# Optimization experiments

Hardware: AMD Instinct MI355X
Metric: run time of the kernel (lower is better)

## Reference

```python
import jax, jax.numpy as jnp
import numpy as np

B = 65536
D_IN = 512
H = 512
EPS = 1e-5


def _layernorm(x, gamma, beta):
    # matches torch ref: unbiased std (ddof=1), eps added to std (not var)
    mean = jnp.mean(x, axis=-1, keepdims=True)
    std = jnp.std(x, axis=-1, ddof=1, keepdims=True)
    return gamma * (x - mean) / (std + EPS) + beta


def setup_inputs() -> dict:
    key = jax.random.key(0)
    ks = jax.random.split(key, 16)
    fan_in = D_IN + H
    s = 1.0 / np.sqrt(fan_in)
    inp = {
        "x": jax.random.normal(ks[0], (B, D_IN), dtype=jnp.float32),
        "prev_h": jax.random.normal(ks[1], (B, H), dtype=jnp.float32),
        "prev_c": jax.random.normal(ks[2], (B, H), dtype=jnp.float32),
        # torch Linear: weight [out, in], bias [out]
        "Wf": jax.random.uniform(ks[3], (H, fan_in), jnp.float32, -s, s),
        "bf": jax.random.uniform(ks[4], (H,), jnp.float32, -s, s),
        "Wi": jax.random.uniform(ks[5], (H, fan_in), jnp.float32, -s, s),
        "bi": jax.random.uniform(ks[6], (H,), jnp.float32, -s, s),
        "Wo": jax.random.uniform(ks[7], (H, fan_in), jnp.float32, -s, s),
        "bo": jax.random.uniform(ks[8], (H,), jnp.float32, -s, s),
        "Wj": jax.random.uniform(ks[9], (H, fan_in), jnp.float32, -s, s),
        "bj": jax.random.uniform(ks[10], (H,), jnp.float32, -s, s),
        "gamma_f": jnp.ones((H,), jnp.float32),
        "beta_f": jnp.zeros((H,), jnp.float32),
        "gamma_i": jnp.ones((H,), jnp.float32),
        "beta_i": jnp.zeros((H,), jnp.float32),
        "gamma_o": jnp.ones((H,), jnp.float32),
        "beta_o": jnp.zeros((H,), jnp.float32),
        "gamma_j": jnp.ones((H,), jnp.float32),
        "beta_j": jnp.zeros((H,), jnp.float32),
        "gamma_c": jnp.ones((H,), jnp.float32),
        "beta_c": jnp.zeros((H,), jnp.float32),
    }
    return inp


def reference(x, prev_h, prev_c, Wf, bf, Wi, bi, Wo, bo, Wj, bj,
              gamma_f, beta_f, gamma_i, beta_i, gamma_o, beta_o,
              gamma_j, beta_j, gamma_c, beta_c):
    combined = jnp.concatenate([x, prev_h], axis=-1)  # [B, D_IN+H]
    ft = jax.nn.sigmoid(_layernorm(combined @ Wf.T + bf, gamma_f, beta_f))
    it = jax.nn.sigmoid(_layernorm(combined @ Wi.T + bi, gamma_i, beta_i))
    ot = jax.nn.sigmoid(_layernorm(combined @ Wo.T + bo, gamma_o, beta_o))
    jt = jnp.tanh(_layernorm(combined @ Wj.T + bj, gamma_j, beta_j))
    c = ft * prev_c + jnp.minimum(1.0 - ft, it) * jt
    c = _layernorm(c, gamma_c, beta_c)
    h = ot * c
    return (h, c)
```

## Files before the change

### kernel.cpp

```cpp
#include <hip/hip_runtime.h>
#include <math.h>

#define B_ROWS 65536
#define D_IN   512
#define HDIM   512
#define FAN    1024
#define NCOL   2048
#define EPS    1e-5f

#define BM 256
#define BN 256
#define BK 64
#define KTILES (FAN / BK)
#define NITER  (KTILES / 2)

typedef unsigned short u16;
using bfrag = __attribute__((ext_vector_type(8))) short;
using facc  = __attribute__((ext_vector_type(4))) float;
using us4   = __attribute__((ext_vector_type(4))) unsigned short;
using us8   = __attribute__((ext_vector_type(8))) unsigned short;

static __device__ __forceinline__ u16 f2b(float f) {
    unsigned u = __builtin_bit_cast(unsigned, f);
    u += 0x7fffu + ((u >> 16) & 1u);
    return (u16)(u >> 16);
}
static __device__ __forceinline__ float b2f(u16 h) {
    unsigned u = ((unsigned)h) << 16;
    return __builtin_bit_cast(float, u);
}
static __device__ __forceinline__ void gload16(const u16* g, u16* l) {
    __builtin_amdgcn_global_load_lds(
        (const __attribute__((address_space(1))) void*)g,
        (__attribute__((address_space(3))) void*)l, 16, 0, 0);
}

__global__ void pack_combined(const float* __restrict__ x, const float* __restrict__ ph,
                              u16* __restrict__ comb)
{
    long i = (long)blockIdx.x * 256 + threadIdx.x;
    if (i >= (long)B_ROWS * D_IN / 4) return;
    long e = i * 4;
    long b = e >> 9;
    int  d = (int)(e & 511);
    float4 xv = *(const float4*)(x + e);
    float4 hv = *(const float4*)(ph + e);
    us4 xb = { f2b(xv.x), f2b(xv.y), f2b(xv.z), f2b(xv.w) };
    us4 hb = { f2b(hv.x), f2b(hv.y), f2b(hv.z), f2b(hv.w) };
    *(us4*)(comb + b * FAN + d)        = xb;
    *(us4*)(comb + b * FAN + D_IN + d) = hb;
}

__global__ void pack_w(const float* __restrict__ Wf, const float* __restrict__ Wi,
                       const float* __restrict__ Wo, const float* __restrict__ Wj,
                       u16* __restrict__ Wall)
{
    long i = (long)blockIdx.x * 256 + threadIdx.x;
    if (i >= (long)NCOL * FAN / 4) return;
    long e = i * 4;
    int  g = (int)(e >> 19);
    long rem = e & 524287L;
    const float* src = (g == 0) ? Wf : (g == 1) ? Wi : (g == 2) ? Wo : Wj;
    float4 v = *(const float4*)(src + rem);
    us4 p = { f2b(v.x), f2b(v.y), f2b(v.z), f2b(v.w) };
    *(us4*)(Wall + e) = p;
}

__global__ __launch_bounds__(512)
void gemm_gates(const u16* __restrict__ A, const u16* __restrict__ W, u16* __restrict__ Cg)
{
    __shared__ u16 lds[2][4][8192];

    const int tid  = threadIdx.x;
    const int lane = tid & 63;
    const int wid  = tid >> 6;
    const int wm   = wid >> 2;
    const int wn   = wid & 3;

    const int nwg = gridDim.x;
    const int wg  = (blockIdx.x & 7) * (nwg >> 3) + (blockIdx.x >> 3);
    const long bm = wg >> 3;
    const int  bn = wg & 7;
    const long arow0 = bm * BM;
    const long bcol0 = (long)bn * BN;

    const int sr = tid >> 3;
    const int ss = tid & 7;

    facc acc[8][4];
#pragma unroll
    for (int i = 0; i < 8; ++i)
#pragma unroll
        for (int j = 0; j < 4; ++j) acc[i][j] = facc{0.f, 0.f, 0.f, 0.f};

    auto stageHalf = [&](int buf, int half, int kt) {
        const long k0 = (long)kt * BK;
#pragma unroll
        for (int i = 0; i < 2; ++i) {
            const int r  = sr + i * 64;
            const int sx = ss ^ (r & 7);
            const u16* src = (half < 2)
                ? (A + (arow0 + half * 128 + r) * (long)FAN + k0 + sx * 8)
                : (W + (bcol0 + (half - 2) * 128 + r) * (long)FAN + k0 + sx * 8);
            gload16(src, &lds[buf][half][i * 4096 + wid * 512]);
        }
    };

    stageHalf(0, 0, 0); stageHalf(0, 1, 0); stageHalf(0, 2, 0); stageHalf(0, 3, 0);
    stageHalf(1, 2, 1); stageHalf(1, 3, 1);
    asm volatile("s_waitcnt vmcnt(4)" ::: "memory");
    __builtin_amdgcn_s_barrier();

    const u16* Ah[2] = { &lds[0][wm][0],            &lds[1][wm][0] };
    const u16* Bh[2] = { &lds[0][2 + (wn >> 1)][0], &lds[1][2 + (wn >> 1)][0] };
    const int lrB0 = (wn & 1) * 64;

#pragma unroll 1
    for (int t = 0; t < NITER; ++t) {
        const bool pf = (t + 1 < NITER);
        bfrag bq[4][2];
#pragma unroll
        for (int p = 0; p < 8; ++p) {
            const int q  = p & 3;
            const int lt = p >> 2;
            bfrag aq[2][2];
            if (q == 0) {
#pragma unroll
                for (int nf = 0; nf < 4; ++nf)
#pragma unroll
                    for (int kk = 0; kk < 2; ++kk) {
                        const int lr = lrB0 + nf * 16 + (lane & 15);
                        const int sl = (kk * 4 + (lane >> 4)) ^ (lane & 7);
                        bq[nf][kk] = *(const bfrag*)(Bh[lt] + lr * 64 + sl * 8);
                    }
            }
#pragma unroll
            for (int m2 = 0; m2 < 2; ++m2)
#pragma unroll
                for (int kk = 0; kk < 2; ++kk) {
                    const int lr = (q * 2 + m2) * 16 + (lane & 15);
                    const int sl = (kk * 4 + (lane >> 4)) ^ (lane & 7);
                    aq[m2][kk] = *(const bfrag*)(Ah[lt] + lr * 64 + sl * 8);
                }
            if (p == 0)      stageHalf(1, 0, 2 * t + 1);
            else if (p == 1) stageHalf(1, 1, 2 * t + 1);
            else if (p == 2) { if (pf) stageHalf(0, 2, 2 * t + 2); }
            else if (p == 3) { if (pf) stageHalf(0, 3, 2 * t + 2); }
            else if (p == 4) { if (pf) stageHalf(0, 0, 2 * t + 2); }
            else if (p == 5) { if (pf) stageHalf(0, 1, 2 * t + 2); }
            else if (p == 6) { if (pf) stageHalf(1, 2, 2 * t + 3); }
            else             { if (pf) stageHalf(1, 3, 2 * t + 3); }

            if (q == 0) asm volatile("s_waitcnt lgkmcnt(8)" ::: "memory");
            __builtin_amdgcn_s_barrier();
            asm volatile("s_waitcnt lgkmcnt(0)" ::: "memory");
            __builtin_amdgcn_s_setprio(1);
#pragma unroll
            for (int m2 = 0; m2 < 2; ++m2)
#pragma unroll
                for (int nf = 0; nf < 4; ++nf)
#pragma unroll
                    for (int kk = 0; kk < 2; ++kk)
                        acc[q * 2 + m2][nf] = __builtin_amdgcn_mfma_f32_16x16x32_bf16(
                            aq[m2][kk], bq[nf][kk], acc[q * 2 + m2][nf], 0, 0, 0);
            __builtin_amdgcn_s_setprio(0);
            if (q == 3) {
                if (pf) asm volatile("s_waitcnt vmcnt(4)" ::: "memory");
                else    asm volatile("s_waitcnt vmcnt(0)" ::: "memory");
            }
            __builtin_amdgcn_s_barrier();
        }
    }

    u16* ct = (u16*)lds;
#pragma unroll
    for (int mf = 0; mf < 8; ++mf)
#pragma unroll
        for (int nf = 0; nf < 4; ++nf) {
            const int row = wm * 128 + mf * 16 + ((lane >> 4) << 2);
            const int col = wn * 64 + nf * 16 + (lane & 15);
#pragma unroll
            for (int r = 0; r < 4; ++r)
                ct[(row + r) * 256 + col] = f2b(acc[mf][nf][r]);
        }
    __syncthreads();
#pragma unroll
    for (int it = 0; it < 16; ++it) {
        const int idx = it * 512 + tid;
        const int row = idx >> 5;
        const int col = (idx & 31) * 8;
        *(us8*)(Cg + (arow0 + row) * (long)NCOL + bcol0 + col) = *(const us8*)(ct + row * 256 + col);
    }
}

static __device__ __forceinline__ void wave_meanrstd(float s, float ss, float& mean, float& rstd)
{
#pragma unroll
    for (int o = 1; o < 64; o <<= 1) { s += __shfl_xor(s, o); ss += __shfl_xor(ss, o); }
    mean = s * (1.f / 512.f);
    float var = (ss - 512.f * mean * mean) * (1.f / 511.f);
    rstd = 1.f / (sqrtf(fmaxf(var, 0.f)) + EPS);
}

__global__ __launch_bounds__(256)
void lstm_act(const u16* __restrict__ pre, const float* __restrict__ pc,
              const float* __restrict__ bf_, const float* __restrict__ bi_,
              const float* __restrict__ bo_, const float* __restrict__ bj_,
              const float* __restrict__ gf, const float* __restrict__ btf,
              const float* __restrict__ gi, const float* __restrict__ bti,
              const float* __restrict__ go, const float* __restrict__ bto,
              const float* __restrict__ gj, const float* __restrict__ btj,
              const float* __restrict__ gc, const float* __restrict__ btc,
              float* __restrict__ out_h, float* __restrict__ out_c)
{
    const long row  = (long)blockIdx.x * 4 + (threadIdx.x >> 6);
    const int  lane = threadIdx.x & 63;
    const int  c0   = lane * 8;

    const float* bs[4]  = { bf_, bi_, bo_, bj_ };
    const float* gs[4]  = { gf, gi, go, gj };
    const float* bts[4] = { btf, bti, bto, btj };

    float a[4][8];
#pragma unroll
    for (int g = 0; g < 4; ++g) {
        us8 pv = *(const us8*)(pre + row * NCOL + g * HDIM + c0);
        float4 bv0 = *(const float4*)(bs[g] + c0);
        float4 bv1 = *(const float4*)(bs[g] + c0 + 4);
        float bb[8] = { bv0.x, bv0.y, bv0.z, bv0.w, bv1.x, bv1.y, bv1.z, bv1.w };
        float y[8];
        float s = 0.f, ssum = 0.f;
#pragma unroll
        for (int e = 0; e < 8; ++e) {
            y[e] = b2f(pv[e]) + bb[e];
            s += y[e]; ssum += y[e] * y[e];
        }
        float mean, rstd;
        wave_meanrstd(s, ssum, mean, rstd);
        float4 g0 = *(const float4*)(gs[g] + c0);
        float4 g1 = *(const float4*)(gs[g] + c0 + 4);
        float4 t0 = *(const float4*)(bts[g] + c0);
        float4 t1 = *(const float4*)(bts[g] + c0 + 4);
        float gg[8] = { g0.x, g0.y, g0.z, g0.w, g1.x, g1.y, g1.z, g1.w };
        float tt[8] = { t0.x, t0.y, t0.z, t0.w, t1.x, t1.y, t1.z, t1.w };
#pragma unroll
        for (int e = 0; e < 8; ++e) {
            float z = (y[e] - mean) * rstd * gg[e] + tt[e];
            a[g][e] = (g == 3) ? tanhf(z) : 1.f / (1.f + expf(-z));
        }
    }

    float4 p0 = *(const float4*)(pc + row * HDIM + c0);
    float4 p1 = *(const float4*)(pc + row * HDIM + c0 + 4);
    float pcv[8] = { p0.x, p0.y, p0.z, p0.w, p1.x, p1.y, p1.z, p1.w };
    float cr[8];
    float s = 0.f, ssum = 0.f;
#pragma unroll
    for (int e = 0; e < 8; ++e) {
        cr[e] = a[0][e] * pcv[e] + fminf(1.f - a[0][e], a[1][e]) * a[3][e];
        s += cr[e]; ssum += cr[e] * cr[e];
    }
    float mean, rstd;
    wave_meanrstd(s, ssum, mean, rstd);
    float4 gc0 = *(const float4*)(gc + c0);
    float4 gc1 = *(const float4*)(gc + c0 + 4);
    float4 tc0 = *(const float4*)(btc + c0);
    float4 tc1 = *(const float4*)(btc + c0 + 4);
    float gg[8] = { gc0.x, gc0.y, gc0.z, gc0.w, gc1.x, gc1.y, gc1.z, gc1.w };
    float tt[8] = { tc0.x, tc0.y, tc0.z, tc0.w, tc1.x, tc1.y, tc1.z, tc1.w };
    float hv[8], cv[8];
#pragma unroll
    for (int e = 0; e < 8; ++e) {
        float cc = (cr[e] - mean) * rstd * gg[e] + tt[e];
        cv[e] = cc;
        hv[e] = a[2][e] * cc;
    }
    *(float4*)(out_h + row * HDIM + c0)     = make_float4(hv[0], hv[1], hv[2], hv[3]);
    *(float4*)(out_h + row * HDIM + c0 + 4) = make_float4(hv[4], hv[5], hv[6], hv[7]);
    *(float4*)(out_c + row * HDIM + c0)     = make_float4(cv[0], cv[1], cv[2], cv[3]);
    *(float4*)(out_c + row * HDIM + c0 + 4) = make_float4(cv[4], cv[5], cv[6], cv[7]);
}

static __device__ __forceinline__ void ln_pair(
    float y0, float y1,
    const float* __restrict__ gam, const float* __restrict__ bet, int c0,
    float* red, int lane, int wid, float& o0, float& o1)
{
    float s = y0 + y1, ss = y0 * y0 + y1 * y1;
#pragma unroll
    for (int o = 32; o; o >>= 1) { s += __shfl_down(s, o); ss += __shfl_down(ss, o); }
    if (lane == 0) { red[wid * 2] = s; red[wid * 2 + 1] = ss; }
    __syncthreads();
    float S  = red[0] + red[2] + red[4] + red[6];
    float SS = red[1] + red[3] + red[5] + red[7];
    __syncthreads();
    float mean = S * (1.f / 512.f);
    float var  = (SS - 512.f * mean * mean) * (1.f / 511.f);
    float rstd = 1.f / (sqrtf(fmaxf(var, 0.f)) + EPS);
    o0 = (y0 - mean) * rstd * gam[c0]     + bet[c0];
    o1 = (y1 - mean) * rstd * gam[c0 + 1] + bet[c0 + 1];
}

__global__ __launch_bounds__(256)
void lstm_naive(const float* __restrict__ x, const float* __restrict__ ph, const float* __restrict__ pc,
                const float* __restrict__ Wf, const float* __restrict__ bf_,
                const float* __restrict__ Wi, const float* __restrict__ bi_,
                const float* __restrict__ Wo, const float* __restrict__ bo_,
                const float* __restrict__ Wj, const float* __restrict__ bj_,
                const float* __restrict__ gf, const float* __restrict__ btf,
                const float* __restrict__ gi, const float* __restrict__ bti,
                const float* __restrict__ go, const float* __restrict__ bto,
                const float* __restrict__ gj, const float* __restrict__ btj,
                const float* __restrict__ gc, const float* __restrict__ btc,
                float* __restrict__ out_h, float* __restrict__ out_c)
{
    __shared__ float comb[FAN];
    __shared__ float red[8];
    const int b = blockIdx.x, t = threadIdx.x;
    const int lane = t & 63, wid = t >> 6;
    for (int k = t; k < D_IN; k += 256) {
        comb[k]        = x[(long)b * D_IN + k];
        comb[D_IN + k] = ph[(long)b * HDIM + k];
    }
    __syncthreads();
    const int c0 = t * 2;
    const float* Ws[4]  = { Wf, Wi, Wo, Wj };
    const float* bs[4]  = { bf_, bi_, bo_, bj_ };
    const float* gs[4]  = { gf, gi, go, gj };
    const float* bts[4] = { btf, bti, bto, btj };
    float a[4][2];
#pragma unroll
    for (int g = 0; g < 4; ++g) {
        float y[2];
#pragma unroll
        for (int e = 0; e < 2; ++e) {
            const float4* w4 = (const float4*)(Ws[g] + (long)(c0 + e) * FAN);
            const float4* c4 = (const float4*)comb;
            float s = 0.f;
            for (int k = 0; k < FAN / 4; ++k) {
                float4 wv = w4[k], cv = c4[k];
                s += wv.x * cv.x + wv.y * cv.y + wv.z * cv.z + wv.w * cv.w;
            }
            y[e] = s + bs[g][c0 + e];
        }
        ln_pair(y[0], y[1], gs[g], bts[g], c0, red, lane, wid, a[g][0], a[g][1]);
        if (g == 3) { a[g][0] = tanhf(a[g][0]); a[g][1] = tanhf(a[g][1]); }
        else        { a[g][0] = 1.f / (1.f + expf(-a[g][0]));
                      a[g][1] = 1.f / (1.f + expf(-a[g][1])); }
    }
    float2 pcv = *(const float2*)(pc + (long)b * HDIM + c0);
    float f0 = a[0][0], i0 = a[1][0], o0 = a[2][0], j0 = a[3][0];
    float f1 = a[0][1], i1 = a[1][1], o1 = a[2][1], j1 = a[3][1];
    float cr0 = f0 * pcv.x + fminf(1.f - f0, i0) * j0;
    float cr1 = f1 * pcv.y + fminf(1.f - f1, i1) * j1;
    float cc0, cc1;
    ln_pair(cr0, cr1, gc, btc, c0, red, lane, wid, cc0, cc1);
    *(float2*)(out_h + (long)b * HDIM + c0) = make_float2(o0 * cc0, o1 * cc1);
    *(float2*)(out_c + (long)b * HDIM + c0) = make_float2(cc0, cc1);
}

extern "C" void kernel_launch(void* const* d_in, const int* in_sizes, int n_in,
                              void* d_out, int out_size, void* d_ws, size_t ws_size,
                              hipStream_t stream)
{
    const float* x   = (const float*)d_in[0];
    const float* ph  = (const float*)d_in[1];
    const float* pc  = (const float*)d_in[2];
    const float* Wf  = (const float*)d_in[3];
    const float* bf_ = (const float*)d_in[4];
    const float* Wi  = (const float*)d_in[5];
    const float* bi_ = (const float*)d_in[6];
    const float* Wo  = (const float*)d_in[7];
    const float* bo_ = (const float*)d_in[8];
    const float* Wj  = (const float*)d_in[9];
    const float* bj_ = (const float*)d_in[10];
    const float* gf  = (const float*)d_in[11];
    const float* btf = (const float*)d_in[12];
    const float* gi  = (const float*)d_in[13];
    const float* bti = (const float*)d_in[14];
    const float* go  = (const float*)d_in[15];
    const float* bto = (const float*)d_in[16];
    const float* gj  = (const float*)d_in[17];
    const float* btj = (const float*)d_in[18];
    const float* gc  = (const float*)d_in[19];
    const float* btc = (const float*)d_in[20];
    float* out_h = (float*)d_out;
    float* out_c = out_h + (size_t)B_ROWS * HDIM;

    const size_t combElems  = (size_t)B_ROWS * FAN;
    const size_t wElems     = (size_t)NCOL * FAN;
    const size_t fixedBytes = (combElems + wElems) * 2;

    long slabRows = 0;
    if (ws_size > fixedBytes) {
        size_t avail = ws_size - fixedBytes;
        slabRows = (long)(avail / ((size_t)NCOL * 2));
        slabRows &= ~255L;
        if (slabRows > B_ROWS) slabRows = B_ROWS;
    }

    if (slabRows >= 256) {
        u16* comb = (u16*)d_ws;
        u16* Wall = comb + combElems;
        u16* pre  = Wall + wElems;
        pack_combined<<<dim3((unsigned)((B_ROWS * (long)D_IN / 4 + 255) / 256)), dim3(256), 0, stream>>>(x, ph, comb);
        pack_w<<<dim3((unsigned)(((long)NCOL * FAN / 4 + 255) / 256)), dim3(256), 0, stream>>>(Wf, Wi, Wo, Wj, Wall);
        for (long r0 = 0; r0 < B_ROWS; r0 += slabRows) {
            long rows = B_ROWS - r0; if (rows > slabRows) rows = slabRows;
            gemm_gates<<<dim3((unsigned)((rows / BM) * (NCOL / BN))), dim3(512), 0, stream>>>(
                comb + r0 * FAN, Wall, pre);
            lstm_act<<<dim3((unsigned)(rows / 4)), dim3(256), 0, stream>>>(
                pre, pc + r0 * HDIM,
                bf_, bi_, bo_, bj_,
                gf, btf, gi, bti, go, bto, gj, btj, gc, btc,
                out_h + r0 * HDIM, out_c + r0 * HDIM);
        }
    } else {
        lstm_naive<<<dim3(B_ROWS), dim3(256), 0, stream>>>(
            x, ph, pc, Wf, bf_, Wi, bi_, Wo, bo_, Wj, bj_,
            gf, btf, gi, bti, go, bto, gj, btj, gc, btc, out_h, out_c);
    }
}
```

Measured before the change: 523.2 us.

## Make GEMM blocks persist over four N tiles and use fast activations

```diff
diff --git a/kernel.cpp b/kernel.cpp
--- a/kernel.cpp
+++ b/kernel.cpp
@@ -13,6 +13,7 @@
 #define BK 64
 #define KTILES (FAN / BK)
 #define NITER  (KTILES / 2)
+#define TILES_PER_BLK 4
 
 typedef unsigned short u16;
 using bfrag = __attribute__((ext_vector_type(8))) short;
@@ -78,11 +79,10 @@
     const int wn   = wid & 3;
 
     const int nwg = gridDim.x;
-    const int wg  = (blockIdx.x & 7) * (nwg >> 3) + (blockIdx.x >> 3);
-    const long bm = wg >> 3;
-    const int  bn = wg & 7;
+    const int swz = (blockIdx.x & 7) * (nwg >> 3) + (blockIdx.x >> 3);
+    const long bm  = swz >> 1;
+    const int  bn4 = (swz & 1) * TILES_PER_BLK;
     const long arow0 = bm * BM;
-    const long bcol0 = (long)bn * BN;
 
     const int sr = tid >> 3;
     const int ss = tid & 7;
@@ -93,8 +93,10 @@
 #pragma unroll
         for (int j = 0; j < 4; ++j) acc[i][j] = facc{0.f, 0.f, 0.f, 0.f};
 
-    auto stageHalf = [&](int buf, int half, int kt) {
-        const long k0 = (long)kt * BK;
+    auto stageHalf = [&](int buf, int half, int ktg) {
+        if (ktg >= TILES_PER_BLK * KTILES) ktg = 0;
+        const long k0    = (long)(ktg & (KTILES - 1)) * BK;
+        const long bcol0 = ((long)bn4 + (ktg >> 4)) * BN;
 #pragma unroll
         for (int i = 0; i < 2; ++i) {
             const int r  = sr + i * 64;
@@ -116,80 +118,73 @@
     const int lrB0 = (wn & 1) * 64;
 
 #pragma unroll 1
-    for (int t = 0; t < NITER; ++t) {
-        const bool pf = (t + 1 < NITER);
-        bfrag bq[4][2];
-#pragma unroll
-        for (int p = 0; p < 8; ++p) {
-            const int q  = p & 3;
-            const int lt = p >> 2;
-            bfrag aq[2][2];
-            if (q == 0) {
-#pragma unroll
-                for (int nf = 0; nf < 4; ++nf)
+    for (int tile = 0; tile < TILES_PER_BLK; ++tile) {
+        const int kb = tile * KTILES;
+#pragma unroll 1
+        for (int t = 0; t < NITER; ++t) {
+            bfrag bq[4][2];
+#pragma unroll
+            for (int p = 0; p < 8; ++p) {
+                const int q  = p & 3;
+                const int lt = p >> 2;
+                bfrag aq[2][2];
+                if (q == 0) {
+#pragma unroll
+                    for (int nf = 0; nf < 4; ++nf)
+#pragma unroll
+                        for (int kk = 0; kk < 2; ++kk) {
+                            const int lr = lrB0 + nf * 16 + (lane & 15);
+                            const int sl = (kk * 4 + (lane >> 4)) ^ (lane & 7);
+                            bq[nf][kk] = *(const bfrag*)(Bh[lt] + lr * 64 + sl * 8);
+                        }
+                }
+#pragma unroll
+                for (int m2 = 0; m2 < 2; ++m2)
 #pragma unroll
                     for (int kk = 0; kk < 2; ++kk) {
-                        const int lr = lrB0 + nf * 16 + (lane & 15);
+                        const int lr = (q * 2 + m2) * 16 + (lane & 15);
                         const int sl = (kk * 4 + (lane >> 4)) ^ (lane & 7);
-                        bq[nf][kk] = *(const bfrag*)(Bh[lt] + lr * 64 + sl * 8);
+                        aq[m2][kk] = *(const bfrag*)(Ah[lt] + lr * 64 + sl * 8);
                     }
+                if (p == 0)      stageHalf(1, 0, kb + 2 * t + 1);
+                else if (p == 1) stageHalf(1, 1, kb + 2 * t + 1);
+                else if (p == 2) stageHalf(0, 2, kb + 2 * t + 2);
+                else if (p == 3) stageHalf(0, 3, kb + 2 * t + 2);
+                else if (p == 4) stageHalf(0, 0, kb + 2 * t + 2);
+                else if (p == 5) stageHalf(0, 1, kb + 2 * t + 2);
+                else if (p == 6) stageHalf(1, 2, kb + 2 * t + 3);
+                else             stageHalf(1, 3, kb + 2 * t + 3);
+
+                if (q == 0) asm volatile("s_waitcnt lgkmcnt(8)" ::: "memory");
+                __builtin_amdgcn_s_barrier();
+                asm volatile("s_waitcnt lgkmcnt(0)" ::: "memory");
+                __builtin_amdgcn_s_setprio(1);
+#pragma unroll
+                for (int m2 = 0; m2 < 2; ++m2)
+#pragma unroll
+                    for (int nf = 0; nf < 4; ++nf)
+#pragma unroll
+                        for (int kk = 0; kk < 2; ++kk)
+                            acc[q * 2 + m2][nf] = __builtin_amdgcn_mfma_f32_16x16x32_bf16(
+                                aq[m2][kk], bq[nf][kk], acc[q * 2 + m2][nf], 0, 0, 0);
+                __builtin_amdgcn_s_setprio(0);
+                if (q == 3) asm volatile("s_waitcnt vmcnt(4)" ::: "memory");
+                __builtin_amdgcn_s_barrier();
             }
-#pragma unroll
-            for (int m2 = 0; m2 < 2; ++m2)
-#pragma unroll
-                for (int kk = 0; kk < 2; ++kk) {
-                    const int lr = (q * 2 + m2) * 16 + (lane & 15);
-                    const int sl = (kk * 4 + (lane >> 4)) ^ (lane & 7);
-                    aq[m2][kk] = *(const bfrag*)(Ah[lt] + lr * 64 + sl * 8);
-                }
-            if (p == 0)      stageHalf(1, 0, 2 * t + 1);
-            else if (p == 1) stageHalf(1, 1, 2 * t + 1);
-            else if (p == 2) { if (pf) stageHalf(0, 2, 2 * t + 2); }
-            else if (p == 3) { if (pf) stageHalf(0, 3, 2 * t + 2); }
-            else if (p == 4) { if (pf) stageHalf(0, 0, 2 * t + 2); }
-            else if (p == 5) { if (pf) stageHalf(0, 1, 2 * t + 2); }
-            else if (p == 6) { if (pf) stageHalf(1, 2, 2 * t + 3); }
-            else             { if (pf) stageHalf(1, 3, 2 * t + 3); }
-
-            if (q == 0) asm volatile("s_waitcnt lgkmcnt(8)" ::: "memory");
-            __builtin_amdgcn_s_barrier();
-            asm volatile("s_waitcnt lgkmcnt(0)" ::: "memory");
-            __builtin_amdgcn_s_setprio(1);
-#pragma unroll
-            for (int m2 = 0; m2 < 2; ++m2)
-#pragma unroll
-                for (int nf = 0; nf < 4; ++nf)
-#pragma unroll
-                    for (int kk = 0; kk < 2; ++kk)
-                        acc[q * 2 + m2][nf] = __builtin_amdgcn_mfma_f32_16x16x32_bf16(
-                            aq[m2][kk], bq[nf][kk], acc[q * 2 + m2][nf], 0, 0, 0);
-            __builtin_amdgcn_s_setprio(0);
-            if (q == 3) {
-                if (pf) asm volatile("s_waitcnt vmcnt(4)" ::: "memory");
-                else    asm volatile("s_waitcnt vmcnt(0)" ::: "memory");
+        }
+
+        const long bcol0 = ((long)bn4 + tile) * BN;
+#pragma unroll
+        for (int mf = 0; mf < 8; ++mf)
+#pragma unroll
+            for (int nf = 0; nf < 4; ++nf) {
+                const long row = arow0 + wm * 128 + mf * 16 + ((lane >> 4) << 2);
+                const long col = bcol0 + wn * 64 + nf * 16 + (lane & 15);
+                u16* p = Cg + row * (long)NCOL + col;
+#pragma unroll
+                for (int r = 0; r < 4; ++r) p[(long)r * NCOL] = f2b(acc[mf][nf][r]);
+                acc[mf][nf] = facc{0.f, 0.f, 0.f, 0.f};
             }
-            __builtin_amdgcn_s_barrier();
-        }
-    }
-
-    u16* ct = (u16*)lds;
-#pragma unroll
-    for (int mf = 0; mf < 8; ++mf)
-#pragma unroll
-        for (int nf = 0; nf < 4; ++nf) {
-            const int row = wm * 128 + mf * 16 + ((lane >> 4) << 2);
-            const int col = wn * 64 + nf * 16 + (lane & 15);
-#pragma unroll
-            for (int r = 0; r < 4; ++r)
-                ct[(row + r) * 256 + col] = f2b(acc[mf][nf][r]);
-        }
-    __syncthreads();
-#pragma unroll
-    for (int it = 0; it < 16; ++it) {
-        const int idx = it * 512 + tid;
-        const int row = idx >> 5;
-        const int col = (idx & 31) * 8;
-        *(us8*)(Cg + (arow0 + row) * (long)NCOL + bcol0 + col) = *(const us8*)(ct + row * 256 + col);
     }
 }
 
@@ -200,6 +195,12 @@
     mean = s * (1.f / 512.f);
     float var = (ss - 512.f * mean * mean) * (1.f / 511.f);
     rstd = 1.f / (sqrtf(fmaxf(var, 0.f)) + EPS);
+}
+static __device__ __forceinline__ float fast_sigmoid(float z) {
+    return __fdividef(1.f, 1.f + __expf(-z));
+}
+static __device__ __forceinline__ float fast_tanh(float z) {
+    return __fdividef(2.f, 1.f + __expf(-2.f * z)) - 1.f;
 }
 
 __global__ __launch_bounds__(256)
@@ -246,7 +247,7 @@
 #pragma unroll
         for (int e = 0; e < 8; ++e) {
             float z = (y[e] - mean) * rstd * gg[e] + tt[e];
-            a[g][e] = (g == 3) ? tanhf(z) : 1.f / (1.f + expf(-z));
+            a[g][e] = (g == 3) ? fast_tanh(z) : fast_sigmoid(z);
         }
     }
 
@@ -395,11 +396,11 @@
     if (ws_size > fixedBytes) {
         size_t avail = ws_size - fixedBytes;
         slabRows = (long)(avail / ((size_t)NCOL * 2));
-        slabRows &= ~255L;
+        slabRows &= ~1023L;
         if (slabRows > B_ROWS) slabRows = B_ROWS;
     }
 
-    if (slabRows >= 256) {
+    if (slabRows >= 1024) {
         u16* comb = (u16*)d_ws;
         u16* Wall = comb + combElems;
         u16* pre  = Wall + wElems;
@@ -407,8 +408,8 @@
         pack_w<<<dim3((unsigned)(((long)NCOL * FAN / 4 + 255) / 256)), dim3(256), 0, stream>>>(Wf, Wi, Wo, Wj, Wall);
         for (long r0 = 0; r0 < B_ROWS; r0 += slabRows) {
             long rows = B_ROWS - r0; if (rows > slabRows) rows = slabRows;
-            gemm_gates<<<dim3((unsigned)((rows / BM) * (NCOL / BN))), dim3(512), 0, stream>>>(
-                comb + r0 * FAN, Wall, pre);
+            const unsigned nwg = (unsigned)((rows / BM) * 2);
+            gemm_gates<<<dim3(nwg), dim3(512), 0, stream>>>(comb + r0 * FAN, Wall, pre);
             lstm_act<<<dim3((unsigned)(rows / 4)), dim3(256), 0, stream>>>(
                 pre, pc + r0 * HDIM,
                 bf_, bi_, bo_, bj_,
```

After: 526.3 us. Within noise of the previous version (+0.6%).
